# Kernel optimization log

Hardware: AMD Instinct MI355X
Metric: run time of the kernel (lower is better)

## Reference

```python
import jax, jax.numpy as jnp
import numpy as np

GRID_MIN, GRID_MAX, GRID_SIZE = -4.0, 4.0, 12
BANDWIDTH = (GRID_MAX - GRID_MIN) / max(GRID_SIZE - 1, 1)  # 8/11


def setup_inputs() -> dict:
    key = jax.random.key(0)
    k1, k2, k3, k4 = jax.random.split(key, 4)
    B, I, O, G = 16384, 512, 512, GRID_SIZE
    x = jax.random.normal(k1, (B, I), dtype=jnp.float32)
    coeff = jax.random.normal(k2, (I, O, G), dtype=jnp.float32) * 0.05
    base_w = jax.random.normal(k3, (O, I), dtype=jnp.float32) * (1.0 / np.sqrt(I))
    base_b = jax.random.normal(k4, (O,), dtype=jnp.float32) * 0.01
    centers = jnp.linspace(GRID_MIN, GRID_MAX, G, dtype=jnp.float32)
    return {"x": x, "coeff": coeff, "base_w": base_w, "base_b": base_b, "centers": centers}


def reference(x, coeff, base_w, base_b, centers):
    # RBF basis: [B, I, G]
    diff = (x[..., None] - centers) / jnp.float32(BANDWIDTH)
    basis = jnp.exp(-0.5 * diff * diff)
    # spline contraction over in_dim and grid: [B, O]
    spline = jnp.einsum('big,iog->bo', basis, coeff)
    # residual base linear (torch Linear: x @ W^T + b)
    return spline + x @ base_w.T + base_b
```

## Files before the change

### kernel.cpp

```cpp
#include <hip/hip_runtime.h>
#include <hip/hip_bf16.h>


#define N_DIM 512
#define I_DIM 512
#define KTOT  6656
#define NSTEP 104

typedef short short8 __attribute__((ext_vector_type(8)));
typedef float f32x16 __attribute__((ext_vector_type(16)));
typedef unsigned int u32x4 __attribute__((ext_vector_type(4)));

#define CVTPK(dst, lo, hi) \
  asm("v_cvt_pk_bf16_f32 %0, %1, %2" : "=v"(dst) : "v"(lo), "v"(hi))

__device__ __forceinline__ unsigned short f2bf(float f) {
  union { float f; unsigned int u; } c; c.f = f;
  unsigned int r = (c.u + 0x7FFFu + ((c.u >> 16) & 1)) >> 16;
  return (unsigned short)r;
}

__global__ __launch_bounds__(256) void prep_w(const float* __restrict__ coeff,
                                              const float* __restrict__ base_w,
                                              unsigned short* __restrict__ Wb2) {
  int t = blockIdx.x * 256 + threadIdx.x;
  int e0 = (t & 1) * 4;
  int go = t >> 1;
  int o  = go & 511;
  int g  = go >> 9;
  int k4 = g * 8 + e0;
  int ic = k4 / 832;
  int rem = k4 - ic * 832;
  int slot = rem >> 6;
  int ii = rem & 63;
  int i = ic * 64 + ii;
  float v0, v1, v2, v3;
  if (slot == 0) {
    const float4 bw = *(const float4*)(base_w + (size_t)o * I_DIM + i);
    v0 = bw.x; v1 = bw.y; v2 = bw.z; v3 = bw.w;
  } else {
    int gg = slot - 1;
    const float* cp = coeff + (size_t)i * (N_DIM * 12) + o * 12 + gg;
    v0 = cp[0]; v1 = cp[6144]; v2 = cp[2 * 6144]; v3 = cp[3 * 6144];
  }
  ushort4 s;
  s.x = f2bf(v0); s.y = f2bf(v1); s.z = f2bf(v2); s.w = f2bf(v3);
  *(ushort4*)(Wb2 + (size_t)go * 8 + e0) = s;
}

__global__ __launch_bounds__(512, 2) void kan_gemm(const float* __restrict__ x,
                                                   const unsigned short* __restrict__ Wb2,
                                                   const float* __restrict__ bias,
                                                   float* __restrict__ out) {
  __shared__ unsigned short Asw[2][8 * 128 * 8];

  const int tid  = threadIdx.x;
  const int lane = tid & 63;
  const int wid  = tid >> 6;
  const int wm   = wid >> 2, wn = wid & 3;
  const int l31  = lane & 31, hl = lane >> 5;

  const int bid = blockIdx.x;
  const int xcd = bid & 7, jj = bid >> 3;
  const int cb  = xcd >> 2;
  const int rb  = jj * 4 + (xcd & 3);
  const int M0  = rb * 128;
  const int N0  = cb * 256;

  const int arow = tid & 127;
  const int kgp  = tid >> 7;
  const float* xg = x + (size_t)(M0 + arow) * I_DIM + kgp * 16;
  const int aoff0 = ((kgp * 2) * 128 + arow) * 16;
  const int aoff1 = ((kgp * 2 + 1) * 128 + arow) * 16;

  const char* Wb = (const char*)Wb2;
  int boff[4][2];
#pragma unroll
  for (int s = 0; s < 4; ++s)
#pragma unroll
    for (int fo = 0; fo < 2; ++fo)
      boff[s][fo] = (((s * 2 + hl) * 512) + N0 + wn * 64 + fo * 32 + l31) * 16;

  const int aBase = (hl * 128 + wm * 64 + l31) * 16;

  f32x16 acc[2][2];
#pragma unroll
  for (int i = 0; i < 2; ++i)
#pragma unroll
    for (int j = 0; j < 2; ++j)
#pragma unroll
      for (int r = 0; r < 16; ++r) acc[i][j][r] = 0.f;

  float bb[16], ff[16];
  float4 xh[4];
  int eslot = 1, cchunk = 0;
#pragma unroll
  for (int q = 0; q < 4; ++q) xh[q] = *(const float4*)(xg + q * 4);

  auto loadB = [&](short8 (&bv)[4][2], int tt) {
    const char* WbT = Wb + (size_t)tt * 65536;
#pragma unroll
    for (int s = 0; s < 4; ++s) {
      bv[s][0] = *(const short8*)(WbT + boff[s][0]);
      bv[s][1] = *(const short8*)(WbT + boff[s][1]);
    }
  };

  auto body = [&](int tt, int abuf, short8 (&bvC)[4][2], short8 (&bvN)[4][2]) {
    if (tt < NSTEP - 1) loadB(bvN, tt + 1);

    const char* pA  = (const char*)&Asw[abuf][0];
    short8 av[4][2];
#pragma unroll
    for (int s = 0; s < 4; ++s) {
      av[s][0] = *(const short8*)(pA + aBase + s * 4096);
      av[s][1] = *(const short8*)(pA + aBase + s * 4096 + 512);
    }

    if (tt < NSTEP - 1) {
      char* pAe = (char*)&Asw[abuf ^ 1][0];
      unsigned int w[8];
      if (eslot == 0) {
        float f[16];
#pragma unroll
        for (int q = 0; q < 4; ++q) {
          f[q*4+0] = xh[q].x; f[q*4+1] = xh[q].y; f[q*4+2] = xh[q].z; f[q*4+3] = xh[q].w;
        }
#pragma unroll
        for (int j = 0; j < 8; ++j) CVTPK(w[j], f[2*j], f[2*j+1]);
        *(u32x4*)(pAe + aoff0) = (u32x4){w[0], w[1], w[2], w[3]};
        *(u32x4*)(pAe + aoff1) = (u32x4){w[4], w[5], w[6], w[7]};
#pragma unroll
        for (int j = 0; j < 16; ++j) {
          float u = fmaf(f[j], 1.375f, 5.5f);
          bb[j] = exp2f(-0.72134752044448170f * u * u);
          ff[j] = exp2f(fmaf(u, 1.44269504088896340f, -0.72134752044448170f));
        }
      } else {
#pragma unroll
        for (int j = 0; j < 8; ++j) CVTPK(w[j], bb[2*j], bb[2*j+1]);
        *(u32x4*)(pAe + aoff0) = (u32x4){w[0], w[1], w[2], w[3]};
        *(u32x4*)(pAe + aoff1) = (u32x4){w[4], w[5], w[6], w[7]};
#pragma unroll
        for (int j = 0; j < 16; ++j) {
          bb[j] *= ff[j];
          ff[j] *= 0.36787944117144233f;
        }
      }
      if (eslot == 1 && cchunk < 7) {
        ++cchunk;
        const float* xn = xg + (size_t)cchunk * 64;
#pragma unroll
        for (int q = 0; q < 4; ++q) xh[q] = *(const float4*)(xn + q * 4);
      }
      eslot = (eslot == 12) ? 0 : eslot + 1;
    }

#pragma unroll
    for (int s = 0; s < 4; ++s) {
      acc[0][0] = __builtin_amdgcn_mfma_f32_32x32x16_bf16(av[s][0], bvC[s][0], acc[0][0], 0, 0, 0);
      acc[0][1] = __builtin_amdgcn_mfma_f32_32x32x16_bf16(av[s][0], bvC[s][1], acc[0][1], 0, 0, 0);
      acc[1][0] = __builtin_amdgcn_mfma_f32_32x32x16_bf16(av[s][1], bvC[s][0], acc[1][0], 0, 0, 0);
      acc[1][1] = __builtin_amdgcn_mfma_f32_32x32x16_bf16(av[s][1], bvC[s][1], acc[1][1], 0, 0, 0);
    }

    asm volatile("s_waitcnt lgkmcnt(0)" ::: "memory");
    __builtin_amdgcn_s_barrier();
  };

  short8 bvA[4][2], bvB[4][2];
  {
    float f[16];
#pragma unroll
    for (int q = 0; q < 4; ++q) {
      f[q*4+0] = xh[q].x; f[q*4+1] = xh[q].y; f[q*4+2] = xh[q].z; f[q*4+3] = xh[q].w;
    }
    unsigned int w[8];
#pragma unroll
    for (int j = 0; j < 8; ++j) CVTPK(w[j], f[2*j], f[2*j+1]);
    char* pAe = (char*)&Asw[0][0];
    *(u32x4*)(pAe + aoff0) = (u32x4){w[0], w[1], w[2], w[3]};
    *(u32x4*)(pAe + aoff1) = (u32x4){w[4], w[5], w[6], w[7]};
#pragma unroll
    for (int j = 0; j < 16; ++j) {
      float u = fmaf(f[j], 1.375f, 5.5f);
      bb[j] = exp2f(-0.72134752044448170f * u * u);
      ff[j] = exp2f(fmaf(u, 1.44269504088896340f, -0.72134752044448170f));
    }
  }
  loadB(bvA, 0);
  asm volatile("s_waitcnt lgkmcnt(0)" ::: "memory");
  __builtin_amdgcn_s_barrier();

#pragma unroll 1
  for (int t = 0; t < NSTEP; t += 2) {
    body(t,     0, bvA, bvB);
    body(t + 1, 1, bvB, bvA);
  }

  float bvv[2];
#pragma unroll
  for (int fo = 0; fo < 2; ++fo) bvv[fo] = bias[N0 + wn * 64 + fo * 32 + l31];
  const int rbase = 4 * hl;
#pragma unroll
  for (int fb = 0; fb < 2; ++fb) {
#pragma unroll
    for (int fo = 0; fo < 2; ++fo) {
      const size_t cix = (size_t)(N0 + wn * 64 + fo * 32 + l31);
#pragma unroll
      for (int r = 0; r < 16; ++r) {
        int row = M0 + wm * 64 + fb * 32 + (r & 3) + 8 * (r >> 2) + rbase;
        out[(size_t)row * N_DIM + cix] = acc[fb][fo][r] + bvv[fo];
      }
    }
  }
}

extern "C" void kernel_launch(void* const* d_in, const int* in_sizes, int n_in,
                              void* d_out, int out_size, void* d_ws, size_t ws_size,
                              hipStream_t stream) {
  const float* x      = (const float*)d_in[0];
  const float* coeff  = (const float*)d_in[1];
  const float* base_w = (const float*)d_in[2];
  const float* base_b = (const float*)d_in[3];
  unsigned short* Wb2 = (unsigned short*)d_ws;

  prep_w<<<3328, 256, 0, stream>>>(coeff, base_w, Wb2);
  kan_gemm<<<256, 512, 0, stream>>>(x, Wb2, base_b, (float*)d_out);
}
```

Baseline: 132.7 us.

## Process two K-steps per barrier with doubled LDS A buffers

Restructures the main loop so each iteration handles two K-steps (a pair) between barriers, doubling the LDS A staging buffer and keeping four B register sets in flight. This halves the number of workgroup barriers and waitcnt drains per K. It raises LDS usage to 64KB per block and increases register pressure from the extra B fragments, which may hurt occupancy at two blocks per CU.

```diff
diff --git a/kernel.cpp b/kernel.cpp
--- a/kernel.cpp
+++ b/kernel.cpp
@@ -6,6 +6,7 @@
 #define I_DIM 512
 #define KTOT  6656
 #define NSTEP 104
+#define NPAIR 52
 
 typedef short short8 __attribute__((ext_vector_type(8)));
 typedef float f32x16 __attribute__((ext_vector_type(16)));
@@ -52,7 +53,7 @@
                                                    const unsigned short* __restrict__ Wb2,
                                                    const float* __restrict__ bias,
                                                    float* __restrict__ out) {
-  __shared__ unsigned short Asw[2][8 * 128 * 8];
+  __shared__ unsigned short Asw[2][2 * 8 * 128 * 8];
 
   const int tid  = threadIdx.x;
   const int lane = tid & 63;
@@ -93,7 +94,7 @@
 
   float bb[16], ff[16];
   float4 xh[4];
-  int eslot = 1, cchunk = 0;
+  int eslot = 0, cchunk = 0;
 #pragma unroll
   for (int q = 0; q < 4; ++q) xh[q] = *(const float4*)(xg + q * 4);
 
@@ -106,96 +107,95 @@
     }
   };
 
-  auto body = [&](int tt, int abuf, short8 (&bvC)[4][2], short8 (&bvN)[4][2]) {
-    if (tt < NSTEP - 1) loadB(bvN, tt + 1);
-
+  auto emitA = [&](char* pDst) {
+    unsigned int w[8];
+    if (eslot == 0) {
+      float f[16];
+#pragma unroll
+      for (int q = 0; q < 4; ++q) {
+        f[q*4+0] = xh[q].x; f[q*4+1] = xh[q].y; f[q*4+2] = xh[q].z; f[q*4+3] = xh[q].w;
+      }
+#pragma unroll
+      for (int j = 0; j < 8; ++j) CVTPK(w[j], f[2*j], f[2*j+1]);
+      *(u32x4*)(pDst + aoff0) = (u32x4){w[0], w[1], w[2], w[3]};
+      *(u32x4*)(pDst + aoff1) = (u32x4){w[4], w[5], w[6], w[7]};
+#pragma unroll
+      for (int j = 0; j < 16; ++j) {
+        float u = fmaf(f[j], 1.375f, 5.5f);
+        bb[j] = exp2f(-0.72134752044448170f * u * u);
+        ff[j] = exp2f(fmaf(u, 1.44269504088896340f, -0.72134752044448170f));
+      }
+    } else {
+#pragma unroll
+      for (int j = 0; j < 8; ++j) CVTPK(w[j], bb[2*j], bb[2*j+1]);
+      *(u32x4*)(pDst + aoff0) = (u32x4){w[0], w[1], w[2], w[3]};
+      *(u32x4*)(pDst + aoff1) = (u32x4){w[4], w[5], w[6], w[7]};
+#pragma unroll
+      for (int j = 0; j < 16; ++j) {
+        bb[j] *= ff[j];
+        ff[j] *= 0.36787944117144233f;
+      }
+    }
+    if (eslot == 1 && cchunk < 7) {
+      ++cchunk;
+      const float* xn = xg + (size_t)cchunk * 64;
+#pragma unroll
+      for (int q = 0; q < 4; ++q) xh[q] = *(const float4*)(xn + q * 4);
+    }
+    eslot = (eslot == 12) ? 0 : eslot + 1;
+  };
+
+#define MFMA_CLUSTER(AV, BV)                                                         \
+  _Pragma("unroll")                                                                  \
+  for (int s = 0; s < 4; ++s) {                                                      \
+    acc[0][0] = __builtin_amdgcn_mfma_f32_32x32x16_bf16(AV[s][0], BV[s][0], acc[0][0], 0, 0, 0); \
+    acc[0][1] = __builtin_amdgcn_mfma_f32_32x32x16_bf16(AV[s][0], BV[s][1], acc[0][1], 0, 0, 0); \
+    acc[1][0] = __builtin_amdgcn_mfma_f32_32x32x16_bf16(AV[s][1], BV[s][0], acc[1][0], 0, 0, 0); \
+    acc[1][1] = __builtin_amdgcn_mfma_f32_32x32x16_bf16(AV[s][1], BV[s][1], acc[1][1], 0, 0, 0); \
+  }
+
+  auto pairBody = [&](int p, int abuf, short8 (&bc0)[4][2], short8 (&bc1)[4][2],
+                      short8 (&bn0)[4][2], short8 (&bn1)[4][2]) {
+    const int t0 = 2 * p;
+    const bool more = (t0 + 2 < NSTEP);
     const char* pA  = (const char*)&Asw[abuf][0];
+    char*       pAe = (char*)&Asw[abuf ^ 1][0];
+
+    if (more) loadB(bn0, t0 + 2);
     short8 av[4][2];
 #pragma unroll
     for (int s = 0; s < 4; ++s) {
       av[s][0] = *(const short8*)(pA + aBase + s * 4096);
       av[s][1] = *(const short8*)(pA + aBase + s * 4096 + 512);
     }
-
-    if (tt < NSTEP - 1) {
-      char* pAe = (char*)&Asw[abuf ^ 1][0];
-      unsigned int w[8];
-      if (eslot == 0) {
-        float f[16];
-#pragma unroll
-        for (int q = 0; q < 4; ++q) {
-          f[q*4+0] = xh[q].x; f[q*4+1] = xh[q].y; f[q*4+2] = xh[q].z; f[q*4+3] = xh[q].w;
-        }
-#pragma unroll
-        for (int j = 0; j < 8; ++j) CVTPK(w[j], f[2*j], f[2*j+1]);
-        *(u32x4*)(pAe + aoff0) = (u32x4){w[0], w[1], w[2], w[3]};
-        *(u32x4*)(pAe + aoff1) = (u32x4){w[4], w[5], w[6], w[7]};
-#pragma unroll
-        for (int j = 0; j < 16; ++j) {
-          float u = fmaf(f[j], 1.375f, 5.5f);
-          bb[j] = exp2f(-0.72134752044448170f * u * u);
-          ff[j] = exp2f(fmaf(u, 1.44269504088896340f, -0.72134752044448170f));
-        }
-      } else {
-#pragma unroll
-        for (int j = 0; j < 8; ++j) CVTPK(w[j], bb[2*j], bb[2*j+1]);
-        *(u32x4*)(pAe + aoff0) = (u32x4){w[0], w[1], w[2], w[3]};
-        *(u32x4*)(pAe + aoff1) = (u32x4){w[4], w[5], w[6], w[7]};
-#pragma unroll
-        for (int j = 0; j < 16; ++j) {
-          bb[j] *= ff[j];
-          ff[j] *= 0.36787944117144233f;
-        }
-      }
-      if (eslot == 1 && cchunk < 7) {
-        ++cchunk;
-        const float* xn = xg + (size_t)cchunk * 64;
-#pragma unroll
-        for (int q = 0; q < 4; ++q) xh[q] = *(const float4*)(xn + q * 4);
-      }
-      eslot = (eslot == 12) ? 0 : eslot + 1;
-    }
-
+    if (more) emitA(pAe);
+    MFMA_CLUSTER(av, bc0);
+
+    if (more) loadB(bn1, t0 + 3);
 #pragma unroll
     for (int s = 0; s < 4; ++s) {
-      acc[0][0] = __builtin_amdgcn_mfma_f32_32x32x16_bf16(av[s][0], bvC[s][0], acc[0][0], 0, 0, 0);
-      acc[0][1] = __builtin_amdgcn_mfma_f32_32x32x16_bf16(av[s][0], bvC[s][1], acc[0][1], 0, 0, 0);
-      acc[1][0] = __builtin_amdgcn_mfma_f32_32x32x16_bf16(av[s][1], bvC[s][0], acc[1][0], 0, 0, 0);
-      acc[1][1] = __builtin_amdgcn_mfma_f32_32x32x16_bf16(av[s][1], bvC[s][1], acc[1][1], 0, 0, 0);
-    }
+      av[s][0] = *(const short8*)(pA + 16384 + aBase + s * 4096);
+      av[s][1] = *(const short8*)(pA + 16384 + aBase + s * 4096 + 512);
+    }
+    if (more) emitA(pAe + 16384);
+    MFMA_CLUSTER(av, bc1);
 
     asm volatile("s_waitcnt lgkmcnt(0)" ::: "memory");
     __builtin_amdgcn_s_barrier();
   };
 
-  short8 bvA[4][2], bvB[4][2];
-  {
-    float f[16];
-#pragma unroll
-    for (int q = 0; q < 4; ++q) {
-      f[q*4+0] = xh[q].x; f[q*4+1] = xh[q].y; f[q*4+2] = xh[q].z; f[q*4+3] = xh[q].w;
-    }
-    unsigned int w[8];
-#pragma unroll
-    for (int j = 0; j < 8; ++j) CVTPK(w[j], f[2*j], f[2*j+1]);
-    char* pAe = (char*)&Asw[0][0];
-    *(u32x4*)(pAe + aoff0) = (u32x4){w[0], w[1], w[2], w[3]};
-    *(u32x4*)(pAe + aoff1) = (u32x4){w[4], w[5], w[6], w[7]};
-#pragma unroll
-    for (int j = 0; j < 16; ++j) {
-      float u = fmaf(f[j], 1.375f, 5.5f);
-      bb[j] = exp2f(-0.72134752044448170f * u * u);
-      ff[j] = exp2f(fmaf(u, 1.44269504088896340f, -0.72134752044448170f));
-    }
-  }
+  short8 bvA[4][2], bvB[4][2], bvC[4][2], bvD[4][2];
+  emitA((char*)&Asw[0][0]);
+  emitA((char*)&Asw[0][0] + 16384);
   loadB(bvA, 0);
+  loadB(bvB, 1);
   asm volatile("s_waitcnt lgkmcnt(0)" ::: "memory");
   __builtin_amdgcn_s_barrier();
 
 #pragma unroll 1
-  for (int t = 0; t < NSTEP; t += 2) {
-    body(t,     0, bvA, bvB);
-    body(t + 1, 1, bvB, bvA);
+  for (int p = 0; p < NPAIR; p += 2) {
+    pairBody(p,     0, bvA, bvB, bvC, bvD);
+    pairBody(p + 1, 1, bvC, bvD, bvA, bvB);
   }
 
   float bvv[2];
```

Result: slower. 258.4 us (+94.8%).
